# Kernel optimization log

Hardware: AMD Instinct MI355X
Metric: run time of the kernel (lower is better)

## Reference

```python
import jax, jax.numpy as jnp
import numpy as np

C = 512      # channels
COND = 256   # cond_dim
H = 8        # n_heads
D = C // H   # head_dim
EPS = 1e-5


def setup_inputs() -> dict:
    key = jax.random.key(0)
    ks = jax.random.split(key, 16)
    s = 0.02
    inp = {
        "x": jax.random.normal(ks[0], (8, C, 1024), jnp.float32),
        "cond": jax.random.normal(ks[1], (8, COND), jnp.float32),
        "ln_g": jnp.ones((C,), jnp.float32),
        "ln_b": jnp.zeros((C,), jnp.float32),
        "Wq": jax.random.normal(ks[2], (C, C), jnp.float32) * s,
        "bq": jnp.zeros((C,), jnp.float32),
        "Wk": jax.random.normal(ks[3], (C, COND), jnp.float32) * s,
        "bk": jnp.zeros((C,), jnp.float32),
        "Wv": jax.random.normal(ks[4], (C, COND), jnp.float32) * s,
        "bv": jnp.zeros((C,), jnp.float32),
        "in_proj_w": jax.random.normal(ks[5], (3 * C, C), jnp.float32) * s,
        "in_proj_b": jnp.zeros((3 * C,), jnp.float32),
        "out_w": jax.random.normal(ks[6], (C, C), jnp.float32) * s,
        "out_b": jnp.zeros((C,), jnp.float32),
        "proj_w": jax.random.normal(ks[7], (C, C), jnp.float32) * s,
        "proj_b": jnp.zeros((C,), jnp.float32),
    }
    return inp


def _forward(x, cond, ln_g, ln_b, Wq, bq, Wk, bk, Wv, bv,
             in_proj_w, in_proj_b, out_w, out_b, proj_w, proj_b):
    B, _, T = x.shape
    x_seq = jnp.transpose(x, (0, 2, 1))                      # [B,T,C]
    mu = jnp.mean(x_seq, axis=-1, keepdims=True)
    var = jnp.mean((x_seq - mu) ** 2, axis=-1, keepdims=True)
    x_norm = (x_seq - mu) / jnp.sqrt(var + EPS) * ln_g + ln_b

    q = x_norm @ Wq.T + bq                                   # [B,T,C]
    k = cond @ Wk.T + bk                                     # [B,C]
    v = cond @ Wv.T + bv                                     # [B,C]

    # nn.MultiheadAttention internal input projections
    wq2, wk2, wv2 = in_proj_w[:C], in_proj_w[C:2 * C], in_proj_w[2 * C:]
    bq2, bk2, bv2 = in_proj_b[:C], in_proj_b[C:2 * C], in_proj_b[2 * C:]
    q2 = q @ wq2.T + bq2                                     # [B,T,C]
    k2 = k @ wk2.T + bk2                                     # [B,C]
    v2 = v @ wv2.T + bv2                                     # [B,C]

    qh = q2.reshape(B, T, H, D)                              # [B,T,H,D]
    kh = k2.reshape(B, H, D)
    vh = v2.reshape(B, H, D)

    # k/v are expanded to length T in the original module -> [B,T,C]
    k_exp = jnp.broadcast_to(kh[:, None, :, :], (B, T, H, D))
    v_exp = jnp.broadcast_to(vh[:, None, :, :], (B, T, H, D))

    scale = 1.0 / jnp.sqrt(jnp.float32(D))
    scores = jnp.einsum('bthd,bshd->bhts', qh * scale, k_exp)  # [B,H,T,T]
    attn = jax.nn.softmax(scores, axis=-1)
    outh = jnp.einsum('bhts,bshd->bthd', attn, v_exp)          # [B,T,H,D]
    out = outh.reshape(B, T, C) @ out_w.T + out_b              # MHA out_proj

    out = out @ proj_w.T + proj_b                              # self.proj
    out = jnp.transpose(out, (0, 2, 1))                        # [B,C,T]
    return x + out


def reference(x, cond, ln_g, ln_b, Wq, bq, Wk, bk, Wv, bv,
              in_proj_w, in_proj_b, out_w, out_b, proj_w, proj_b):
    return _forward(x, cond, ln_g, ln_b, Wq, bq, Wk, bk, Wv, bv,
                    in_proj_w, in_proj_b, out_w, out_b, proj_w, proj_b)
```

## Files before the change

### kernel.cpp

```cpp
#include <hip/hip_runtime.h>

#define CC 512
#define CK 256
#define BB 8
#define TT 1024
#define MAGIC1 0x517E0001u
#define MAGIC2 0x517E0002u

__device__ __forceinline__ float wave_allreduce(float v) {
#pragma unroll
    for (int m = 1; m < 64; m <<= 1) v += __shfl_xor(v, m, 64);
    return v;
}
__device__ __forceinline__ float dot4(float4 a, float4 b) {
    return a.x * b.x + a.y * b.y + a.z * b.z + a.w * b.w;
}

__global__ void __launch_bounds__(512)
chain_kernel(const float* __restrict__ cond,
             const float* __restrict__ Wv, const float* __restrict__ bv,
             const float* __restrict__ W2, const float* __restrict__ b2,
             const float* __restrict__ O,  const float* __restrict__ ob,
             float* __restrict__ v1g, float* __restrict__ v2g,
             float* __restrict__ u, unsigned* __restrict__ slots)
{
    __shared__ float lds[BB * CC];
    const int tid  = threadIdx.x;
    const int lane = tid & 63;
    const int c    = blockIdx.x * 8 + (tid >> 6);
    float accs[BB];

    const float4 wv4 = *(const float4*)&Wv[c * CK + lane * 4];
    const float bvc = bv[c];
#pragma unroll
    for (int b = 0; b < BB; ++b)
        accs[b] = dot4(wv4, *(const float4*)&cond[b * CK + lane * 4]);
#pragma unroll
    for (int b = 0; b < BB; ++b) {
        const float r = wave_allreduce(accs[b]);
        if (lane == 0)
            __hip_atomic_store(&v1g[b * CC + c], r + bvc, __ATOMIC_RELAXED,
                               __HIP_MEMORY_SCOPE_AGENT);
    }
    __syncthreads();
    if (tid == 0) {
        asm volatile("s_waitcnt vmcnt(0)" ::: "memory");
        __hip_atomic_store(&slots[blockIdx.x], MAGIC1, __ATOMIC_RELAXED,
                           __HIP_MEMORY_SCOPE_AGENT);
    }
    const float4 w2a = *(const float4*)&W2[c * CC + lane * 4];
    const float4 w2b = *(const float4*)&W2[c * CC + CK + lane * 4];
    const float b2c = b2[c];
    {
        unsigned* sp = &slots[tid & 63];
        while (__hip_atomic_load(sp, __ATOMIC_RELAXED,
                                 __HIP_MEMORY_SCOPE_AGENT) != MAGIC1)
            __builtin_amdgcn_s_sleep(1);
    }
    asm volatile("" ::: "memory");
    {
        const float4* g4 = (const float4*)v1g;
        float4* l4 = (float4*)lds;
        l4[tid * 2] = g4[tid * 2];
        l4[tid * 2 + 1] = g4[tid * 2 + 1];
    }
    __syncthreads();

#pragma unroll
    for (int b = 0; b < BB; ++b)
        accs[b] = dot4(w2a, *(const float4*)&lds[b * CC + lane * 4]) +
                  dot4(w2b, *(const float4*)&lds[b * CC + CK + lane * 4]);
#pragma unroll
    for (int b = 0; b < BB; ++b) {
        const float r = wave_allreduce(accs[b]);
        if (lane == 0)
            __hip_atomic_store(&v2g[b * CC + c], r + b2c, __ATOMIC_RELAXED,
                               __HIP_MEMORY_SCOPE_AGENT);
    }
    __syncthreads();
    if (tid == 0) {
        asm volatile("s_waitcnt vmcnt(0)" ::: "memory");
        __hip_atomic_store(&slots[64 + blockIdx.x], MAGIC2, __ATOMIC_RELAXED,
                           __HIP_MEMORY_SCOPE_AGENT);
    }
    const float4 oa = *(const float4*)&O[c * CC + lane * 4];
    const float4 oc = *(const float4*)&O[c * CC + CK + lane * 4];
    const float obc = ob[c];
    {
        unsigned* sp = &slots[64 + (tid & 63)];
        while (__hip_atomic_load(sp, __ATOMIC_RELAXED,
                                 __HIP_MEMORY_SCOPE_AGENT) != MAGIC2)
            __builtin_amdgcn_s_sleep(1);
    }
    asm volatile("" ::: "memory");
    {
        const float4* g4 = (const float4*)v2g;
        float4* l4 = (float4*)lds;
        l4[tid * 2] = g4[tid * 2];
        l4[tid * 2 + 1] = g4[tid * 2 + 1];
    }
    __syncthreads();

#pragma unroll
    for (int b = 0; b < BB; ++b)
        accs[b] = dot4(oa, *(const float4*)&lds[b * CC + lane * 4]) +
                  dot4(oc, *(const float4*)&lds[b * CC + CK + lane * 4]);
#pragma unroll
    for (int b = 0; b < BB; ++b) {
        const float r = wave_allreduce(accs[b]);
        if (lane == 0) u[b * CC + c] = r + obc;
    }
}

__global__ void __launch_bounds__(256)
stream_kernel(const float* __restrict__ x, const float* __restrict__ P,
              const float* __restrict__ pb, const float* __restrict__ u,
              unsigned* __restrict__ slots, float* __restrict__ out)
{
    const int tid = threadIdx.x;
    const int lane = tid & 63;
    const int row = blockIdx.x * 4 + (tid >> 6);
    const int b = row >> 9, c = row & 511;
    if (blockIdx.x == 0 && tid < 128) slots[tid] = 0;

    const float4 pa = *(const float4*)&P[c * CC + lane * 4];
    const float4 pc = *(const float4*)&P[c * CC + CK + lane * 4];
    const float4 ua = *(const float4*)&u[b * CC + lane * 4];
    const float4 ub = *(const float4*)&u[b * CC + CK + lane * 4];
    const float w = wave_allreduce(dot4(pa, ua) + dot4(pc, ub)) + pb[c];

    const float4* x4 = (const float4*)x + (size_t)row * (TT / 4);
    float4* o4 = (float4*)out + (size_t)row * (TT / 4);
#pragma unroll
    for (int i = 0; i < 4; ++i) {
        float4 v = x4[i * 64 + lane];
        v.x += w; v.y += w; v.z += w; v.w += w;
        o4[i * 64 + lane] = v;
    }
}

extern "C" void kernel_launch(void* const* d_in, const int* in_sizes, int n_in,
                              void* d_out, int out_size, void* d_ws, size_t ws_size,
                              hipStream_t stream) {
    const float* x    = (const float*)d_in[0];
    const float* cond = (const float*)d_in[1];
    const float* Wv   = (const float*)d_in[8];
    const float* bv   = (const float*)d_in[9];
    const float* W2   = (const float*)d_in[10] + 2 * CC * CC;
    const float* b2   = (const float*)d_in[11] + 2 * CC;
    const float* O    = (const float*)d_in[12];
    const float* ob   = (const float*)d_in[13];
    const float* P    = (const float*)d_in[14];
    const float* pb   = (const float*)d_in[15];
    float* out = (float*)d_out;

    float* v1g = (float*)d_ws;
    float* v2g = v1g + BB * CC;
    float* u   = v2g + BB * CC;
    unsigned* slots = (unsigned*)(u + BB * CC);

    chain_kernel<<<64, 512, 0, stream>>>(cond, Wv, bv, W2, b2, O, ob,
                                         v1g, v2g, u, slots);
    stream_kernel<<<1024, 256, 0, stream>>>(x, P, pb, u, slots, out);
}
```

Baseline: 25.68 us.

## Fuse cond chain and streaming add into one kernel with flag handoff

Merges the small matvec chain and the broadcast-add streaming kernel into one 1024-block launch. The first 64 blocks compute the three chained projections, two channels per wave, and publish a third flag. All blocks prefetch their x rows and P weights, then spin on that flag before finishing the final projection and the add. Flags are padded to separate cache lines and reset by a tiny extra kernel. The goal is to overlap the chain latency with x loads and remove a serialized kernel boundary. In exchange it relies on the producer blocks being scheduled alongside the spinning blocks, and adds an extra launch for the reset.

```diff
diff --git a/kernel.cpp b/kernel.cpp
--- a/kernel.cpp
+++ b/kernel.cpp
@@ -4,8 +4,11 @@
 #define CK 256
 #define BB 8
 #define TT 1024
-#define MAGIC1 0x517E0001u
-#define MAGIC2 0x517E0002u
+#define NPROD 64
+#define SSTR 32
+#define MA 0x517E0001u
+#define MB 0x517E0002u
+#define MC 0x517E0003u
 
 __device__ __forceinline__ float wave_allreduce(float v) {
 #pragma unroll
@@ -15,125 +18,172 @@
 __device__ __forceinline__ float dot4(float4 a, float4 b) {
     return a.x * b.x + a.y * b.y + a.z * b.z + a.w * b.w;
 }
-
-__global__ void __launch_bounds__(512)
-chain_kernel(const float* __restrict__ cond,
+__device__ __forceinline__ void st_agent(float* p, float v) {
+    __hip_atomic_store(p, v, __ATOMIC_RELAXED, __HIP_MEMORY_SCOPE_AGENT);
+}
+__device__ __forceinline__ float ld_agent(const float* p) {
+    return __hip_atomic_load(p, __ATOMIC_RELAXED, __HIP_MEMORY_SCOPE_AGENT);
+}
+__device__ __forceinline__ void st_flag(unsigned* p, unsigned v) {
+    __hip_atomic_store(p, v, __ATOMIC_RELAXED, __HIP_MEMORY_SCOPE_AGENT);
+}
+__device__ __forceinline__ unsigned ld_flag(const unsigned* p) {
+    return __hip_atomic_load(p, __ATOMIC_RELAXED, __HIP_MEMORY_SCOPE_AGENT);
+}
+
+__global__ void __launch_bounds__(256)
+reset_kernel(unsigned* __restrict__ slots) {
+    if (threadIdx.x < 192) st_flag(&slots[threadIdx.x * SSTR], 0u);
+}
+
+__global__ void __launch_bounds__(256)
+fused_kernel(const float* __restrict__ x, const float* __restrict__ cond,
              const float* __restrict__ Wv, const float* __restrict__ bv,
              const float* __restrict__ W2, const float* __restrict__ b2,
              const float* __restrict__ O,  const float* __restrict__ ob,
+             const float* __restrict__ P,  const float* __restrict__ pb,
              float* __restrict__ v1g, float* __restrict__ v2g,
-             float* __restrict__ u, unsigned* __restrict__ slots)
+             float* __restrict__ ug, unsigned* __restrict__ slots,
+             float* __restrict__ out)
 {
     __shared__ float lds[BB * CC];
-    const int tid  = threadIdx.x;
-    const int lane = tid & 63;
-    const int c    = blockIdx.x * 8 + (tid >> 6);
-    float accs[BB];
-
-    const float4 wv4 = *(const float4*)&Wv[c * CK + lane * 4];
-    const float bvc = bv[c];
-#pragma unroll
-    for (int b = 0; b < BB; ++b)
-        accs[b] = dot4(wv4, *(const float4*)&cond[b * CK + lane * 4]);
-#pragma unroll
-    for (int b = 0; b < BB; ++b) {
-        const float r = wave_allreduce(accs[b]);
-        if (lane == 0)
-            __hip_atomic_store(&v1g[b * CC + c], r + bvc, __ATOMIC_RELAXED,
-                               __HIP_MEMORY_SCOPE_AGENT);
+    const int tid = threadIdx.x, lane = tid & 63, wvid = tid >> 6;
+    const int row = blockIdx.x * 4 + wvid;
+    const int rb = row >> 9, rc = row & 511;
+
+    if (blockIdx.x < NPROD) {
+        const int c0 = (blockIdx.x * 4 + wvid) * 2;
+        {
+            const float4 wva = *(const float4*)&Wv[(size_t)c0 * CK + lane * 4];
+            const float4 wvb = *(const float4*)&Wv[(size_t)(c0 + 1) * CK + lane * 4];
+            const float bva = bv[c0], bvb = bv[c0 + 1];
+            float a0[BB], a1[BB];
+#pragma unroll
+            for (int b = 0; b < BB; ++b) {
+                const float4 cd = *(const float4*)&cond[b * CK + lane * 4];
+                a0[b] = dot4(wva, cd);
+                a1[b] = dot4(wvb, cd);
+            }
+#pragma unroll
+            for (int b = 0; b < BB; ++b) {
+                const float r0 = wave_allreduce(a0[b]);
+                const float r1 = wave_allreduce(a1[b]);
+                if (lane == 0) {
+                    st_agent(&v1g[b * CC + c0], r0 + bva);
+                    st_agent(&v1g[b * CC + c0 + 1], r1 + bvb);
+                }
+            }
+        }
+        __syncthreads();
+        if (tid == 0) {
+            asm volatile("s_waitcnt vmcnt(0)" ::: "memory");
+            st_flag(&slots[blockIdx.x * SSTR], MA);
+        }
+        const float4 w2a0 = *(const float4*)&W2[(size_t)c0 * CC + lane * 4];
+        const float4 w2a1 = *(const float4*)&W2[(size_t)c0 * CC + CK + lane * 4];
+        const float4 w2b0 = *(const float4*)&W2[(size_t)(c0 + 1) * CC + lane * 4];
+        const float4 w2b1 = *(const float4*)&W2[(size_t)(c0 + 1) * CC + CK + lane * 4];
+        const float b2a = b2[c0], b2b = b2[c0 + 1];
+        __builtin_amdgcn_sched_barrier(0);
+        {
+            const unsigned* sp = &slots[(tid & 63) * SSTR];
+            while (ld_flag(sp) != MA) __builtin_amdgcn_s_sleep(1);
+        }
+        asm volatile("" ::: "memory");
+        __syncthreads();
+#pragma unroll
+        for (int i = 0; i < 16; ++i)
+            lds[tid + i * 256] = ld_agent(&v1g[tid + i * 256]);
+        __syncthreads();
+        {
+            float a0[BB], a1[BB];
+#pragma unroll
+            for (int b = 0; b < BB; ++b) {
+                const float4 va = *(const float4*)&lds[b * CC + lane * 4];
+                const float4 vb = *(const float4*)&lds[b * CC + CK + lane * 4];
+                a0[b] = dot4(w2a0, va) + dot4(w2a1, vb);
+                a1[b] = dot4(w2b0, va) + dot4(w2b1, vb);
+            }
+#pragma unroll
+            for (int b = 0; b < BB; ++b) {
+                const float r0 = wave_allreduce(a0[b]);
+                const float r1 = wave_allreduce(a1[b]);
+                if (lane == 0) {
+                    st_agent(&v2g[b * CC + c0], r0 + b2a);
+                    st_agent(&v2g[b * CC + c0 + 1], r1 + b2b);
+                }
+            }
+        }
+        __syncthreads();
+        if (tid == 0) {
+            asm volatile("s_waitcnt vmcnt(0)" ::: "memory");
+            st_flag(&slots[(64 + blockIdx.x) * SSTR], MB);
+        }
+        const float4 oa0 = *(const float4*)&O[(size_t)c0 * CC + lane * 4];
+        const float4 oa1 = *(const float4*)&O[(size_t)c0 * CC + CK + lane * 4];
+        const float4 ob0 = *(const float4*)&O[(size_t)(c0 + 1) * CC + lane * 4];
+        const float4 ob1 = *(const float4*)&O[(size_t)(c0 + 1) * CC + CK + lane * 4];
+        const float oba = ob[c0], obb = ob[c0 + 1];
+        __builtin_amdgcn_sched_barrier(0);
+        {
+            const unsigned* sp = &slots[(64 + (tid & 63)) * SSTR];
+            while (ld_flag(sp) != MB) __builtin_amdgcn_s_sleep(1);
+        }
+        asm volatile("" ::: "memory");
+        __syncthreads();
+#pragma unroll
+        for (int i = 0; i < 16; ++i)
+            lds[tid + i * 256] = ld_agent(&v2g[tid + i * 256]);
+        __syncthreads();
+        {
+            float a0[BB], a1[BB];
+#pragma unroll
+            for (int b = 0; b < BB; ++b) {
+                const float4 va = *(const float4*)&lds[b * CC + lane * 4];
+                const float4 vb = *(const float4*)&lds[b * CC + CK + lane * 4];
+                a0[b] = dot4(oa0, va) + dot4(oa1, vb);
+                a1[b] = dot4(ob0, va) + dot4(ob1, vb);
+            }
+#pragma unroll
+            for (int b = 0; b < BB; ++b) {
+                const float r0 = wave_allreduce(a0[b]);
+                const float r1 = wave_allreduce(a1[b]);
+                if (lane == 0) {
+                    st_agent(&ug[b * CC + c0], r0 + oba);
+                    st_agent(&ug[b * CC + c0 + 1], r1 + obb);
+                }
+            }
+        }
+        __syncthreads();
+        if (tid == 0) {
+            asm volatile("s_waitcnt vmcnt(0)" ::: "memory");
+            st_flag(&slots[(128 + blockIdx.x) * SSTR], MC);
+        }
     }
-    __syncthreads();
-    if (tid == 0) {
-        asm volatile("s_waitcnt vmcnt(0)" ::: "memory");
-        __hip_atomic_store(&slots[blockIdx.x], MAGIC1, __ATOMIC_RELAXED,
-                           __HIP_MEMORY_SCOPE_AGENT);
-    }
-    const float4 w2a = *(const float4*)&W2[c * CC + lane * 4];
-    const float4 w2b = *(const float4*)&W2[c * CC + CK + lane * 4];
-    const float b2c = b2[c];
+
+    const float4* x4 = (const float4*)x + (size_t)row * (TT / 4);
+    float4 xr[4];
+#pragma unroll
+    for (int i = 0; i < 4; ++i) xr[i] = x4[i * 64 + lane];
+    float pr[8];
+#pragma unroll
+    for (int i = 0; i < 8; ++i) pr[i] = P[(size_t)rc * CC + i * 64 + lane];
+    const float pbc = pb[rc];
+    __builtin_amdgcn_sched_barrier(0);
     {
-        unsigned* sp = &slots[tid & 63];
-        while (__hip_atomic_load(sp, __ATOMIC_RELAXED,
-                                 __HIP_MEMORY_SCOPE_AGENT) != MAGIC1)
-            __builtin_amdgcn_s_sleep(1);
+        const unsigned* sp = &slots[(128 + (tid & 63)) * SSTR];
+        while (ld_flag(sp) != MC) __builtin_amdgcn_s_sleep(2);
     }
     asm volatile("" ::: "memory");
-    {
-        const float4* g4 = (const float4*)v1g;
-        float4* l4 = (float4*)lds;
-        l4[tid * 2] = g4[tid * 2];
-        l4[tid * 2 + 1] = g4[tid * 2 + 1];
-    }
-    __syncthreads();
-
-#pragma unroll
-    for (int b = 0; b < BB; ++b)
-        accs[b] = dot4(w2a, *(const float4*)&lds[b * CC + lane * 4]) +
-                  dot4(w2b, *(const float4*)&lds[b * CC + CK + lane * 4]);
-#pragma unroll
-    for (int b = 0; b < BB; ++b) {
-        const float r = wave_allreduce(accs[b]);
-        if (lane == 0)
-            __hip_atomic_store(&v2g[b * CC + c], r + b2c, __ATOMIC_RELAXED,
-                               __HIP_MEMORY_SCOPE_AGENT);
-    }
-    __syncthreads();
-    if (tid == 0) {
-        asm volatile("s_waitcnt vmcnt(0)" ::: "memory");
-        __hip_atomic_store(&slots[64 + blockIdx.x], MAGIC2, __ATOMIC_RELAXED,
-                           __HIP_MEMORY_SCOPE_AGENT);
-    }
-    const float4 oa = *(const float4*)&O[c * CC + lane * 4];
-    const float4 oc = *(const float4*)&O[c * CC + CK + lane * 4];
-    const float obc = ob[c];
-    {
-        unsigned* sp = &slots[64 + (tid & 63)];
-        while (__hip_atomic_load(sp, __ATOMIC_RELAXED,
-                                 __HIP_MEMORY_SCOPE_AGENT) != MAGIC2)
-            __builtin_amdgcn_s_sleep(1);
-    }
-    asm volatile("" ::: "memory");
-    {
-        const float4* g4 = (const float4*)v2g;
-        float4* l4 = (float4*)lds;
-        l4[tid * 2] = g4[tid * 2];
-        l4[tid * 2 + 1] = g4[tid * 2 + 1];
-    }
-    __syncthreads();
-
-#pragma unroll
-    for (int b = 0; b < BB; ++b)
-        accs[b] = dot4(oa, *(const float4*)&lds[b * CC + lane * 4]) +
-                  dot4(oc, *(const float4*)&lds[b * CC + CK + lane * 4]);
-#pragma unroll
-    for (int b = 0; b < BB; ++b) {
-        const float r = wave_allreduce(accs[b]);
-        if (lane == 0) u[b * CC + c] = r + obc;
-    }
-}
-
-__global__ void __launch_bounds__(256)
-stream_kernel(const float* __restrict__ x, const float* __restrict__ P,
-              const float* __restrict__ pb, const float* __restrict__ u,
-              unsigned* __restrict__ slots, float* __restrict__ out)
-{
-    const int tid = threadIdx.x;
-    const int lane = tid & 63;
-    const int row = blockIdx.x * 4 + (tid >> 6);
-    const int b = row >> 9, c = row & 511;
-    if (blockIdx.x == 0 && tid < 128) slots[tid] = 0;
-
-    const float4 pa = *(const float4*)&P[c * CC + lane * 4];
-    const float4 pc = *(const float4*)&P[c * CC + CK + lane * 4];
-    const float4 ua = *(const float4*)&u[b * CC + lane * 4];
-    const float4 ub = *(const float4*)&u[b * CC + CK + lane * 4];
-    const float w = wave_allreduce(dot4(pa, ua) + dot4(pc, ub)) + pb[c];
-
-    const float4* x4 = (const float4*)x + (size_t)row * (TT / 4);
+    float acc = 0.f;
+#pragma unroll
+    for (int i = 0; i < 8; ++i)
+        acc += pr[i] * ld_agent(&ug[rb * CC + i * 64 + lane]);
+    const float w = wave_allreduce(acc) + pbc;
     float4* o4 = (float4*)out + (size_t)row * (TT / 4);
 #pragma unroll
     for (int i = 0; i < 4; ++i) {
-        float4 v = x4[i * 64 + lane];
+        float4 v = xr[i];
         v.x += w; v.y += w; v.z += w; v.w += w;
         o4[i * 64 + lane] = v;
     }
@@ -156,10 +206,10 @@
 
     float* v1g = (float*)d_ws;
     float* v2g = v1g + BB * CC;
-    float* u   = v2g + BB * CC;
-    unsigned* slots = (unsigned*)(u + BB * CC);
-
-    chain_kernel<<<64, 512, 0, stream>>>(cond, Wv, bv, W2, b2, O, ob,
-                                         v1g, v2g, u, slots);
-    stream_kernel<<<1024, 256, 0, stream>>>(x, P, pb, u, slots, out);
-}
+    float* ug  = v2g + BB * CC;
+    unsigned* slots = (unsigned*)(ug + BB * CC);
+
+    reset_kernel<<<1, 256, 0, stream>>>(slots);
+    fused_kernel<<<1024, 256, 0, stream>>>(x, cond, Wv, bv, W2, b2, O, ob,
+                                           P, pb, v1g, v2g, ug, slots, out);
+}
```

Result: slower. 60.73 us (+136.5%).
